# Optimization experiments

Hardware: AMD Instinct MI355X
Metric: run time of the kernel (lower is better)

Reference implementation:

```python
import jax, jax.numpy as jnp
import numpy as np

HALFKP = 64 * 5 * 64          # 20480
PAD = HALFKP                  # padding row index
L1, L2, L3 = 256, 31, 32
NB = 8                        # layer-stack / psqt buckets
EMB_DIM = L1 + NB             # 264


def setup_inputs() -> dict:
    key = jax.random.key(0)
    ks = jax.random.split(key, 16)
    B = 16384
    w_idx = jax.random.randint(ks[0], (B, 32), 0, HALFKP + 1)
    b_idx = jax.random.randint(ks[1], (B, 32), 0, HALFKP + 1)
    us = jax.random.uniform(ks[2], (B,), dtype=jnp.float32)
    them = jax.random.uniform(ks[3], (B,), dtype=jnp.float32)
    piece_count = jax.random.randint(ks[4], (B,), 2, 33)
    sigma = 0.025
    emb = jax.random.uniform(ks[5], (HALFKP + 1, EMB_DIM), jnp.float32, -sigma, sigma)
    emb = emb.at[PAD].set(0.0)
    def lin(k, out_f, in_f):
        bound = 1.0 / np.sqrt(in_f)
        k1, k2 = jax.random.split(k)
        W = jax.random.uniform(k1, (out_f, in_f), jnp.float32, -bound, bound)
        b = jax.random.uniform(k2, (out_f,), jnp.float32, -bound, bound)
        return W, b
    # StackedLinear init: replicate slot-0 weights across all buckets
    w1_0, b1_0 = lin(ks[6], L2 + 1, L1)
    w1 = jnp.tile(w1_0, (NB, 1)); b1 = jnp.tile(b1_0, NB)
    fw1 = jnp.zeros((L2 + 1, L1), jnp.float32)
    fb1 = jnp.zeros((L2 + 1,), jnp.float32)
    w2_0, b2_0 = lin(ks[7], L3, L2 * 2)
    w2 = jnp.tile(w2_0, (NB, 1)); b2 = jnp.tile(b2_0, NB)
    wo_0, _ = lin(ks[8], 1, L3)
    wo = jnp.tile(wo_0, (NB, 1)); bo = jnp.zeros((NB,), jnp.float32)
    return {"emb": emb, "w1": w1, "b1": b1, "fw1": fw1, "fb1": fb1,
            "w2": w2, "b2": b2, "wo": wo, "bo": bo,
            "us": us, "them": them,
            "w_idx": w_idx, "b_idx": b_idx, "piece_count": piece_count}


def reference(emb, w1, b1, fw1, fb1, w2, b2, wo, bo, us, them,
              w_idx, b_idx, piece_count):
    emb_eff = emb.at[PAD].set(0.0)                      # padding row contributes 0
    wp = emb_eff[w_idx].sum(axis=1)                     # [B, 264]
    bp = emb_eff[b_idx].sum(axis=1)
    w, wpsqt = wp[:, :L1], wp[:, L1:]
    b, bpsqt = bp[:, :L1], bp[:, L1:]
    us_c = us[:, None]; them_c = them[:, None]
    l0 = us_c * jnp.concatenate([w, b], 1) + them_c * jnp.concatenate([b, w], 1)
    l0 = jnp.clip(l0, 0.0, 1.0)                         # [B, 512]
    h = L1 // 2
    l0 = jnp.concatenate([l0[:, :h] * l0[:, h:2*h],
                          l0[:, 2*h:3*h] * l0[:, 3*h:]], 1) * (127.0 / 128.0)  # [B,256]
    bucket = jnp.clip((piece_count - 1) // 4, 0, 7)     # [B]
    # l1: factorized stacked linear, gather the bucket's slice only
    W1 = (w1 + jnp.tile(fw1, (NB, 1))).reshape(NB, L2 + 1, L1)
    B1 = (b1 + jnp.tile(fb1, NB)).reshape(NB, L2 + 1)
    l1c = jnp.einsum('bi,bji->bj', l0, W1[bucket]) + B1[bucket]   # [B,32]
    l1x, l1x_out = l1c[:, :L2], l1c[:, L2:]
    l1x = jnp.clip(jnp.concatenate([l1x * l1x * (255.0 / 256.0), l1x], 1), 0.0, 1.0)  # [B,62]
    W2 = w2.reshape(NB, L3, L2 * 2)
    l2x = jnp.clip(jnp.einsum('bi,bji->bj', l1x, W2[bucket]) + b2.reshape(NB, L3)[bucket], 0.0, 1.0)
    Wo = wo.reshape(NB, 1, L3)
    l3c = jnp.einsum('bi,bji->bj', l2x, Wo[bucket]) + bo.reshape(NB, 1)[bucket]       # [B,1]
    fc_out = l3c + l1x_out
    bk = bucket[:, None]
    psqt_out = (jnp.take_along_axis(wpsqt, bk, 1) - jnp.take_along_axis(bpsqt, bk, 1)) * (us_c - 0.5)
    return fc_out + psqt_out                            # [B,1]
```

## Files before the change

### kernel.cpp

```cpp
#include <hip/hip_runtime.h>

#define EMBD 264
#define NROWS 20481
#define NR4   5121
#define QS 5080.0f
#define INVQS (1.0f/5080.0f)

typedef short short8 __attribute__((ext_vector_type(8)));
typedef float f32x4  __attribute__((ext_vector_type(4)));

__device__ __forceinline__ float clamp01(float x) { return fminf(fmaxf(x, 0.f), 1.f); }
__device__ __forceinline__ unsigned short f2bf(float f) {
    unsigned u = __float_as_uint(f);
    u += 0x7fffu + ((u >> 16) & 1u);
    return (unsigned short)(u >> 16);
}

__global__ void prep_all(const float* __restrict__ emb, unsigned int* __restrict__ emb8,
                         float* __restrict__ psqt,
                         const float* __restrict__ w1, const float* __restrict__ fw1,
                         const float* __restrict__ b1, const float* __restrict__ fb1,
                         const float* __restrict__ w2,
                         unsigned short* __restrict__ w1b, float* __restrict__ b1c,
                         float* __restrict__ w2p) {
    if (blockIdx.x < NR4) {
        const int r = blockIdx.x * 4 + (threadIdx.x >> 6);
        const int t = threadIdx.x & 63;
        if (r >= NROWS) return;
        const bool pad = (r == NROWS - 1);
        const float4 v = *((const float4*)(emb + (size_t)r * EMBD) + t);
        int q0 = pad ? 128 : (int)rintf(v.x * QS) + 128;
        int q1 = pad ? 128 : (int)rintf(v.y * QS) + 128;
        int q2 = pad ? 128 : (int)rintf(v.z * QS) + 128;
        int q3 = pad ? 128 : (int)rintf(v.w * QS) + 128;
        q0 = min(max(q0, 0), 255); q1 = min(max(q1, 0), 255);
        q2 = min(max(q2, 0), 255); q3 = min(max(q3, 0), 255);
        emb8[(size_t)r * 64 + t] = (unsigned)q0 | ((unsigned)q1 << 8) |
                                   ((unsigned)q2 << 16) | ((unsigned)q3 << 24);
        if (t < 8) {
            float pv = emb[(size_t)r * EMBD + 256 + t];
            psqt[r * 8 + t] = pad ? 0.f : pv;
        }
    } else {
        const int e = (blockIdx.x - NR4) * 256 + threadIdx.x;
        const int bkt = e >> 13, rem = e & 8191;
        const int s = rem >> 10, rem2 = rem & 1023;
        const int nt = rem2 >> 9, rem3 = rem2 & 511;
        const int ln = rem3 >> 3, j = rem3 & 7;
        const int n  = nt * 16 + (ln & 15);
        const int hi = ln >> 4;
        const int k  = s * 32 + hi * 8 + j;
        const float v = w1[(bkt * 32 + n) * 256 + k] + fw1[n * 256 + k];
        w1b[e] = f2bf(v);
        if (e < 256) b1c[e] = b1[e] + fb1[e & 31];
        if (e < 16384) {
            const int jr = e >> 6, i = e & 63;
            float x = 0.f;
            if (i < 31) x = w2[jr * 62 + i];
            else if (i >= 32 && i < 63) x = w2[jr * 62 + i - 1];
            w2p[e] = x;
        }
    }
}

__global__ __launch_bounds__(512, 4) void nnue_fwd_mfma(
    const unsigned int* __restrict__ emb8,
    const float* __restrict__ psqt,
    const unsigned short* __restrict__ w1b,
    const float* __restrict__ b1c,
    const float* __restrict__ w2p,
    const float* __restrict__ b2,
    const float* __restrict__ wo,
    const float* __restrict__ bo,
    const float* __restrict__ us,
    const float* __restrict__ them,
    const int*   __restrict__ w_idx,
    const int*   __restrict__ b_idx,
    const int*   __restrict__ pcnt,
    float* __restrict__ out,
    int B)
{
    __shared__ unsigned short A_lds[16 * 280];
    __shared__ float l1c[8 * 16 * 36];
    __shared__ float psq_lds[16];
    __shared__ int   bkt_lds[16];

    const int tid  = threadIdx.x;
    const int lane = tid & 63;
    const int w    = tid >> 6;

    for (int rr = 0; rr < 2; ++rr) {
        const int m = w * 2 + rr;
        const int grow = __builtin_amdgcn_readfirstlane(blockIdx.x * 16 + m);

        const float usv = us[grow];
        const float thv = them[grow];
        int bucket = (pcnt[grow] - 1) >> 2;
        bucket = bucket > 7 ? 7 : bucket;
        bucket = __builtin_amdgcn_readfirstlane(bucket);

        const int* wrow = w_idx + grow * 32;
        const int* brow = b_idx + grow * 32;

        const int kk = lane & 31;
        const int pidx = (lane < 32) ? wrow[kk] : brow[kk];
        float ps = psqt[pidx * 8 + bucket];

        const unsigned M = 0x00FF00FFu;
        const unsigned loff = (unsigned)(lane << 2);
        const char* ebase = (const char*)emb8;

        unsigned vw[32], vb[32];
#pragma unroll
        for (int k = 0; k < 32; ++k) {
            const unsigned iw = (unsigned)__builtin_amdgcn_readfirstlane(wrow[k]);
            vw[k] = *(const unsigned*)(ebase + (size_t)((iw << 8) + loff));
        }
#pragma unroll
        for (int k = 0; k < 32; ++k) {
            const unsigned ib = (unsigned)__builtin_amdgcn_readfirstlane(brow[k]);
            vb[k] = *(const unsigned*)(ebase + (size_t)((ib << 8) + loff));
        }

        unsigned aw0a = 0, aw1a = 0, aw0b = 0, aw1b = 0;
#pragma unroll
        for (int k = 0; k < 32; k += 2) {
            aw0a += vw[k] & M;     aw1a += (vw[k] >> 8) & M;
            aw0b += vw[k+1] & M;   aw1b += (vw[k+1] >> 8) & M;
        }
        unsigned ab0a = 0, ab1a = 0, ab0b = 0, ab1b = 0;
#pragma unroll
        for (int k = 0; k < 32; k += 2) {
            ab0a += vb[k] & M;     ab1a += (vb[k] >> 8) & M;
            ab0b += vb[k+1] & M;   ab1b += (vb[k+1] >> 8) & M;
        }
        const unsigned aw0 = aw0a + aw0b, aw1 = aw1a + aw1b;
        const unsigned ab0 = ab0a + ab0b, ab1 = ab1a + ab1b;

        ps += __shfl_xor(ps, 16);
        ps += __shfl_xor(ps, 8);
        ps += __shfl_xor(ps, 4);
        ps += __shfl_xor(ps, 2);
        ps += __shfl_xor(ps, 1);
        const float psq_w = __shfl(ps, 0);
        const float psq_b = __shfl(ps, 32);

        float4 aw4, ab4;
        aw4.x = ((int)(aw0 & 0xffffu) - 4096) * INVQS;
        aw4.y = ((int)(aw1 & 0xffffu) - 4096) * INVQS;
        aw4.z = ((int)(aw0 >> 16)     - 4096) * INVQS;
        aw4.w = ((int)(aw1 >> 16)     - 4096) * INVQS;
        ab4.x = ((int)(ab0 & 0xffffu) - 4096) * INVQS;
        ab4.y = ((int)(ab1 & 0xffffu) - 4096) * INVQS;
        ab4.z = ((int)(ab0 >> 16)     - 4096) * INVQS;
        ab4.w = ((int)(ab1 >> 16)     - 4096) * INVQS;

        float4 p, q;
        p.x = clamp01(usv * aw4.x + thv * ab4.x);
        p.y = clamp01(usv * aw4.y + thv * ab4.y);
        p.z = clamp01(usv * aw4.z + thv * ab4.z);
        p.w = clamp01(usv * aw4.w + thv * ab4.w);
        q.x = clamp01(usv * ab4.x + thv * aw4.x);
        q.y = clamp01(usv * ab4.y + thv * aw4.y);
        q.z = clamp01(usv * ab4.z + thv * aw4.z);
        q.w = clamp01(usv * ab4.w + thv * aw4.w);

        float4 po, qo;
        po.x = __shfl_xor(p.x, 32); po.y = __shfl_xor(p.y, 32);
        po.z = __shfl_xor(p.z, 32); po.w = __shfl_xor(p.w, 32);
        qo.x = __shfl_xor(q.x, 32); qo.y = __shfl_xor(q.y, 32);
        qo.z = __shfl_xor(q.z, 32); qo.w = __shfl_xor(q.w, 32);
        const float c127 = 127.f / 128.f;
        float4 l0f;
        if (lane < 32) {
            l0f.x = p.x * po.x * c127; l0f.y = p.y * po.y * c127;
            l0f.z = p.z * po.z * c127; l0f.w = p.w * po.w * c127;
        } else {
            l0f.x = q.x * qo.x * c127; l0f.y = q.y * qo.y * c127;
            l0f.z = q.z * qo.z * c127; l0f.w = q.w * qo.w * c127;
        }

        const unsigned lo  = (unsigned)f2bf(l0f.x) | ((unsigned)f2bf(l0f.y) << 16);
        const unsigned hi2 = (unsigned)f2bf(l0f.z) | ((unsigned)f2bf(l0f.w) << 16);
        *((unsigned long long*)&A_lds[m * 280 + lane * 4]) =
            ((unsigned long long)hi2 << 32) | (unsigned long long)lo;
        if (lane == 0) {
            psq_lds[m] = (psq_w - psq_b) * (usv - 0.5f);
            bkt_lds[m] = bucket;
        }
    }
    __syncthreads();

    {
        const int col = lane & 15;
        const int hi  = lane >> 4;
        const int bkt = w;
        f32x4 acc[2];
        acc[0] = (f32x4){0.f, 0.f, 0.f, 0.f};
        acc[1] = (f32x4){0.f, 0.f, 0.f, 0.f};

#pragma unroll
        for (int s = 0; s < 8; ++s) {
            const short8 a = *((const short8*)&A_lds[col * 280 + s * 32 + hi * 8]);
#pragma unroll
            for (int nt = 0; nt < 2; ++nt) {
                const short8 bf = *((const short8*)&w1b[(((bkt * 8 + s) * 2 + nt) * 64 + lane) * 8]);
                acc[nt] = __builtin_amdgcn_mfma_f32_16x16x32_bf16(a, bf, acc[nt], 0, 0, 0);
            }
        }
#pragma unroll
        for (int nt = 0; nt < 2; ++nt) {
            const float bias = b1c[bkt * 32 + nt * 16 + col];
#pragma unroll
            for (int reg = 0; reg < 4; ++reg) {
                const int mr = hi * 4 + reg;
                l1c[(bkt * 16 + mr) * 36 + nt * 16 + col] = acc[nt][reg] + bias;
            }
        }
    }
    __syncthreads();

    if (tid < 256) {
        const int row = tid >> 4;
        const int jj  = tid & 15;
        const int bkt = bkt_lds[row];
        const float4* crow = (const float4*)&l1c[(bkt * 16 + row) * 36];
        float4 c4[8];
#pragma unroll
        for (int b5 = 0; b5 < 8; ++b5) c4[b5] = crow[b5];

        const float4* wr0 = (const float4*)&w2p[(bkt * 32 + jj) * 64];
        const float4* wr1 = (const float4*)&w2p[(bkt * 32 + jj + 16) * 64];
        float acc0 = 0.f, acc1 = 0.f;
        const float kq = 255.f / 256.f;
#pragma unroll
        for (int b5 = 0; b5 < 8; ++b5) {
            const float4 cv = c4[b5];
            float4 sq, ln;
            sq.x = clamp01(cv.x * cv.x * kq); ln.x = clamp01(cv.x);
            sq.y = clamp01(cv.y * cv.y * kq); ln.y = clamp01(cv.y);
            sq.z = clamp01(cv.z * cv.z * kq); ln.z = clamp01(cv.z);
            sq.w = clamp01(cv.w * cv.w * kq); ln.w = clamp01(cv.w);
            const float4 ws0 = wr0[b5], wl0 = wr0[8 + b5];
            const float4 ws1 = wr1[b5], wl1 = wr1[8 + b5];
            acc0 += sq.x * ws0.x + sq.y * ws0.y + sq.z * ws0.z + sq.w * ws0.w;
            acc0 += ln.x * wl0.x + ln.y * wl0.y + ln.z * wl0.z + ln.w * wl0.w;
            acc1 += sq.x * ws1.x + sq.y * ws1.y + sq.z * ws1.z + sq.w * ws1.w;
            acc1 += ln.x * wl1.x + ln.y * wl1.y + ln.z * wl1.z + ln.w * wl1.w;
        }
        const float t0 = clamp01(acc0 + b2[bkt * 32 + jj])      * wo[bkt * 32 + jj];
        const float t1 = clamp01(acc1 + b2[bkt * 32 + jj + 16]) * wo[bkt * 32 + jj + 16];
        float t = t0 + t1;
        t += __shfl_xor(t, 8);
        t += __shfl_xor(t, 4);
        t += __shfl_xor(t, 2);
        t += __shfl_xor(t, 1);
        if (jj == 0) {
            out[blockIdx.x * 16 + row] = t + bo[bkt] + c4[7].w + psq_lds[row];
        }
    }
}

__global__ __launch_bounds__(256) void nnue_fwd_f32(
    const float* __restrict__ emb,
    const float* __restrict__ w1e, const float* __restrict__ fw1,
    const float* __restrict__ b1e, const float* __restrict__ fb1,
    const float* __restrict__ w2,  const float* __restrict__ b2,
    const float* __restrict__ wo,  const float* __restrict__ bo,
    const float* __restrict__ us,  const float* __restrict__ them,
    const int* __restrict__ w_idx, const int* __restrict__ b_idx,
    const int* __restrict__ pcnt,  float* __restrict__ out, int B)
{
    const int lane = threadIdx.x & 63;
    const int row  = blockIdx.x * 4 + (threadIdx.x >> 6);
    if (row >= B) return;
    const float usv = us[row];
    const float thv = them[row];
    int bucket = (pcnt[row] - 1) >> 2;
    bucket = bucket > 7 ? 7 : bucket;
    bucket = __builtin_amdgcn_readfirstlane(bucket);
    const int kk = lane & 31;
    const int myidx = (lane < 32) ? w_idx[row * 32 + kk] : b_idx[row * 32 + kk];
    float ps = emb[(size_t)myidx * EMBD + 256 + bucket];
    ps += __shfl_xor(ps, 16); ps += __shfl_xor(ps, 8);
    ps += __shfl_xor(ps, 4);  ps += __shfl_xor(ps, 2); ps += __shfl_xor(ps, 1);
    const float psq_w = __shfl(ps, 0);
    const float psq_b = __shfl(ps, 32);
    float4 aw = make_float4(0,0,0,0), ab = make_float4(0,0,0,0);
#pragma unroll
    for (int k = 0; k < 32; ++k) {
        const int iw = __shfl(myidx, k);
        const int ib = __shfl(myidx, 32 + k);
        const float4 vw = *((const float4*)(emb + (size_t)iw * EMBD) + lane);
        const float4 vb = *((const float4*)(emb + (size_t)ib * EMBD) + lane);
        aw.x += vw.x; aw.y += vw.y; aw.z += vw.z; aw.w += vw.w;
        ab.x += vb.x; ab.y += vb.y; ab.z += vb.z; ab.w += vb.w;
    }
    float4 p, q;
    p.x = clamp01(usv*aw.x + thv*ab.x); p.y = clamp01(usv*aw.y + thv*ab.y);
    p.z = clamp01(usv*aw.z + thv*ab.z); p.w = clamp01(usv*aw.w + thv*ab.w);
    q.x = clamp01(usv*ab.x + thv*aw.x); q.y = clamp01(usv*ab.y + thv*aw.y);
    q.z = clamp01(usv*ab.z + thv*aw.z); q.w = clamp01(usv*ab.w + thv*aw.w);
    float4 po, qo;
    po.x = __shfl_xor(p.x,32); po.y = __shfl_xor(p.y,32);
    po.z = __shfl_xor(p.z,32); po.w = __shfl_xor(p.w,32);
    qo.x = __shfl_xor(q.x,32); qo.y = __shfl_xor(q.y,32);
    qo.z = __shfl_xor(q.z,32); qo.w = __shfl_xor(q.w,32);
    const float c127 = 127.f/128.f;
    float4 l0f;
    if (lane < 32) { l0f.x=p.x*po.x*c127; l0f.y=p.y*po.y*c127; l0f.z=p.z*po.z*c127; l0f.w=p.w*po.w*c127; }
    else           { l0f.x=q.x*qo.x*c127; l0f.y=q.y*qo.y*c127; l0f.z=q.z*qo.z*c127; l0f.w=q.w*qo.w*c127; }
    float part[32];
    const float4* w1p = (const float4*)(w1e + (size_t)bucket * 8192);
    const float4* f1p = (const float4*)fw1;
#pragma unroll
    for (int j = 0; j < 32; ++j) {
        float4 wv = w1p[j*64 + lane];
        float4 fv = f1p[j*64 + lane];
        wv.x+=fv.x; wv.y+=fv.y; wv.z+=fv.z; wv.w+=fv.w;
        part[j] = l0f.x*wv.x + l0f.y*wv.y + l0f.z*wv.z + l0f.w*wv.w;
    }
#pragma unroll
    for (int j = 0; j < 32; ++j) {
        float v = part[j];
        v += __shfl_xor(v,32); v += __shfl_xor(v,16); v += __shfl_xor(v,8);
        v += __shfl_xor(v,4);  v += __shfl_xor(v,2);  v += __shfl_xor(v,1);
        part[j] = v + b1e[bucket*32 + j] + fb1[j];
    }
    const float l1x_out = part[31];
    float acc2 = 0.f;
    if (lane < 32) {
        const float* w2r = w2 + (size_t)(bucket*32 + lane) * 62;
#pragma unroll
        for (int i = 0; i < 31; ++i) {
            const float a = part[i];
            acc2 += clamp01(a*a*(255.f/256.f)) * w2r[i];
            acc2 += clamp01(a) * w2r[31+i];
        }
        acc2 += b2[bucket*32 + lane];
        acc2 = clamp01(acc2) * wo[bucket*32 + lane];
    }
    acc2 += __shfl_xor(acc2,16); acc2 += __shfl_xor(acc2,8);
    acc2 += __shfl_xor(acc2,4);  acc2 += __shfl_xor(acc2,2); acc2 += __shfl_xor(acc2,1);
    if (lane == 0)
        out[row] = acc2 + bo[bucket] + l1x_out + (psq_w - psq_b) * (usv - 0.5f);
}

extern "C" void kernel_launch(void* const* d_in, const int* in_sizes, int n_in,
                              void* d_out, int out_size, void* d_ws, size_t ws_size,
                              hipStream_t stream) {
    const float* emb  = (const float*)d_in[0];
    const float* w1   = (const float*)d_in[1];
    const float* b1   = (const float*)d_in[2];
    const float* fw1  = (const float*)d_in[3];
    const float* fb1  = (const float*)d_in[4];
    const float* w2   = (const float*)d_in[5];
    const float* b2   = (const float*)d_in[6];
    const float* wo   = (const float*)d_in[7];
    const float* bo   = (const float*)d_in[8];
    const float* us   = (const float*)d_in[9];
    const float* them = (const float*)d_in[10];
    const int*   wi   = (const int*)d_in[11];
    const int*   bi   = (const int*)d_in[12];
    const int*   pc   = (const int*)d_in[13];
    float* out = (float*)d_out;

    const int B = in_sizes[9];

    const size_t emb8_bytes = (size_t)NROWS * 256;
    const size_t psqt_bytes = (size_t)NROWS * 8 * 4;
    const size_t w1b_bytes  = 65536 * 2;
    const size_t b1c_bytes  = 256 * 4;
    const size_t w2p_bytes  = 16384 * 4;
    const size_t need = emb8_bytes + psqt_bytes + w1b_bytes + b1c_bytes + w2p_bytes;

    if (ws_size >= need && (B % 16) == 0) {
        char* p = (char*)d_ws;
        unsigned int*   emb8 = (unsigned int*)p;     p += emb8_bytes;
        float*          psqt = (float*)p;            p += psqt_bytes;
        unsigned short* w1b  = (unsigned short*)p;   p += w1b_bytes;
        float*          b1c  = (float*)p;            p += b1c_bytes;
        float*          w2p  = (float*)p;

        prep_all<<<NR4 + 256, 256, 0, stream>>>(emb, emb8, psqt,
                                                w1, fw1, b1, fb1, w2, w1b, b1c, w2p);
        nnue_fwd_mfma<<<B / 16, 512, 0, stream>>>(emb8, psqt, w1b, b1c, w2p,
                                                  b2, wo, bo, us, them, wi, bi, pc, out, B);
    } else {
        nnue_fwd_f32<<<(B + 3) / 4, 256, 0, stream>>>(emb, w1, fw1, b1, fb1,
                                                      w2, b2, wo, bo, us, them, wi, bi, pc, out, B);
    }
}
```

Measured before the change: 139.5 us.

## Gather embedding rows with 16-byte loads split across lane groups

Replaces 64 scalar 4-byte gathers per row (one per feature, all lanes on one embedding row) with 16 vectorized 16-byte loads. Each 16-lane group fetches a different feature row, and partial sums are then reduced across groups with cross-lane shuffles. This cuts the number of load instructions and the number of readfirstlane index reads. The l0 pairing shuffle and the LDS store index are remapped to the new lane-to-element layout. In exchange it adds shuffle-reduction and select overhead.

```diff
diff --git a/kernel.cpp b/kernel.cpp
--- a/kernel.cpp
+++ b/kernel.cpp
@@ -89,6 +89,10 @@
     const int lane = tid & 63;
     const int w    = tid >> 6;
 
+    const int t = lane & 15;
+    const int g = lane >> 4;
+    const int d = (t << 2) + g;
+
     for (int rr = 0; rr < 2; ++rr) {
         const int m = w * 2 + rr;
         const int grow = __builtin_amdgcn_readfirstlane(blockIdx.x * 16 + m);
@@ -103,39 +107,54 @@
         const int* brow = b_idx + grow * 32;
 
         const int kk = lane & 31;
-        const int pidx = (lane < 32) ? wrow[kk] : brow[kk];
-        float ps = psqt[pidx * 8 + bucket];
+        const int iv = (lane < 32) ? wrow[kk] : brow[kk];
+
+        float ps = psqt[(size_t)iv * 8 + bucket];
+
+        uint4 vws[8], vbs[8];
+#pragma unroll
+        for (int k = 0; k < 8; ++k) {
+            const int rw = __shfl(iv, (k << 2) + g);
+            vws[k] = *(const uint4*)((const char*)emb8 +
+                                     (((unsigned)rw << 8) + (unsigned)(t << 4)));
+        }
+#pragma unroll
+        for (int k = 0; k < 8; ++k) {
+            const int rb = __shfl(iv, 32 + (k << 2) + g);
+            vbs[k] = *(const uint4*)((const char*)emb8 +
+                                     (((unsigned)rb << 8) + (unsigned)(t << 4)));
+        }
 
         const unsigned M = 0x00FF00FFu;
-        const unsigned loff = (unsigned)(lane << 2);
-        const char* ebase = (const char*)emb8;
-
-        unsigned vw[32], vb[32];
-#pragma unroll
-        for (int k = 0; k < 32; ++k) {
-            const unsigned iw = (unsigned)__builtin_amdgcn_readfirstlane(wrow[k]);
-            vw[k] = *(const unsigned*)(ebase + (size_t)((iw << 8) + loff));
-        }
-#pragma unroll
-        for (int k = 0; k < 32; ++k) {
-            const unsigned ib = (unsigned)__builtin_amdgcn_readfirstlane(brow[k]);
-            vb[k] = *(const unsigned*)(ebase + (size_t)((ib << 8) + loff));
-        }
-
-        unsigned aw0a = 0, aw1a = 0, aw0b = 0, aw1b = 0;
-#pragma unroll
-        for (int k = 0; k < 32; k += 2) {
-            aw0a += vw[k] & M;     aw1a += (vw[k] >> 8) & M;
-            aw0b += vw[k+1] & M;   aw1b += (vw[k+1] >> 8) & M;
-        }
-        unsigned ab0a = 0, ab1a = 0, ab0b = 0, ab1b = 0;
-#pragma unroll
-        for (int k = 0; k < 32; k += 2) {
-            ab0a += vb[k] & M;     ab1a += (vb[k] >> 8) & M;
-            ab0b += vb[k+1] & M;   ab1b += (vb[k+1] >> 8) & M;
-        }
-        const unsigned aw0 = aw0a + aw0b, aw1 = aw1a + aw1b;
-        const unsigned ab0 = ab0a + ab0b, ab1 = ab1a + ab1b;
+        unsigned a0w[4] = {0,0,0,0}, a1w[4] = {0,0,0,0};
+        unsigned a0b[4] = {0,0,0,0}, a1b[4] = {0,0,0,0};
+#pragma unroll
+        for (int k = 0; k < 8; ++k) {
+            a0w[0] += vws[k].x & M;  a1w[0] += (vws[k].x >> 8) & M;
+            a0w[1] += vws[k].y & M;  a1w[1] += (vws[k].y >> 8) & M;
+            a0w[2] += vws[k].z & M;  a1w[2] += (vws[k].z >> 8) & M;
+            a0w[3] += vws[k].w & M;  a1w[3] += (vws[k].w >> 8) & M;
+        }
+#pragma unroll
+        for (int k = 0; k < 8; ++k) {
+            a0b[0] += vbs[k].x & M;  a1b[0] += (vbs[k].x >> 8) & M;
+            a0b[1] += vbs[k].y & M;  a1b[1] += (vbs[k].y >> 8) & M;
+            a0b[2] += vbs[k].z & M;  a1b[2] += (vbs[k].z >> 8) & M;
+            a0b[3] += vbs[k].w & M;  a1b[3] += (vbs[k].w >> 8) & M;
+        }
+
+#pragma unroll
+        for (int j = 0; j < 4; ++j) {
+            a0w[j] += __shfl_xor(a0w[j], 16);  a0w[j] += __shfl_xor(a0w[j], 32);
+            a1w[j] += __shfl_xor(a1w[j], 16);  a1w[j] += __shfl_xor(a1w[j], 32);
+            a0b[j] += __shfl_xor(a0b[j], 16);  a0b[j] += __shfl_xor(a0b[j], 32);
+            a1b[j] += __shfl_xor(a1b[j], 16);  a1b[j] += __shfl_xor(a1b[j], 32);
+        }
+        const bool gl = (g & 1) != 0, gh = (g & 2) != 0;
+        const unsigned aw0 = gh ? (gl ? a0w[3] : a0w[2]) : (gl ? a0w[1] : a0w[0]);
+        const unsigned aw1 = gh ? (gl ? a1w[3] : a1w[2]) : (gl ? a1w[1] : a1w[0]);
+        const unsigned ab0 = gh ? (gl ? a0b[3] : a0b[2]) : (gl ? a0b[1] : a0b[0]);
+        const unsigned ab1 = gh ? (gl ? a1b[3] : a1b[2]) : (gl ? a1b[1] : a1b[0]);
 
         ps += __shfl_xor(ps, 16);
         ps += __shfl_xor(ps, 8);
@@ -166,13 +185,13 @@
         q.w = clamp01(usv * ab4.w + thv * aw4.w);
 
         float4 po, qo;
-        po.x = __shfl_xor(p.x, 32); po.y = __shfl_xor(p.y, 32);
-        po.z = __shfl_xor(p.z, 32); po.w = __shfl_xor(p.w, 32);
-        qo.x = __shfl_xor(q.x, 32); qo.y = __shfl_xor(q.y, 32);
-        qo.z = __shfl_xor(q.z, 32); qo.w = __shfl_xor(q.w, 32);
+        po.x = __shfl_xor(p.x, 8); po.y = __shfl_xor(p.y, 8);
+        po.z = __shfl_xor(p.z, 8); po.w = __shfl_xor(p.w, 8);
+        qo.x = __shfl_xor(q.x, 8); qo.y = __shfl_xor(q.y, 8);
+        qo.z = __shfl_xor(q.z, 8); qo.w = __shfl_xor(q.w, 8);
         const float c127 = 127.f / 128.f;
         float4 l0f;
-        if (lane < 32) {
+        if (t < 8) {
             l0f.x = p.x * po.x * c127; l0f.y = p.y * po.y * c127;
             l0f.z = p.z * po.z * c127; l0f.w = p.w * po.w * c127;
         } else {
@@ -182,7 +201,7 @@
 
         const unsigned lo  = (unsigned)f2bf(l0f.x) | ((unsigned)f2bf(l0f.y) << 16);
         const unsigned hi2 = (unsigned)f2bf(l0f.z) | ((unsigned)f2bf(l0f.w) << 16);
-        *((unsigned long long*)&A_lds[m * 280 + lane * 4]) =
+        *((unsigned long long*)&A_lds[m * 280 + d * 4]) =
             ((unsigned long long)hi2 << 32) | (unsigned long long)lo;
         if (lane == 0) {
             psq_lds[m] = (psq_w - psq_b) * (usv - 0.5f);
@@ -250,13 +269,13 @@
         }
         const float t0 = clamp01(acc0 + b2[bkt * 32 + jj])      * wo[bkt * 32 + jj];
         const float t1 = clamp01(acc1 + b2[bkt * 32 + jj + 16]) * wo[bkt * 32 + jj + 16];
-        float t = t0 + t1;
-        t += __shfl_xor(t, 8);
-        t += __shfl_xor(t, 4);
-        t += __shfl_xor(t, 2);
-        t += __shfl_xor(t, 1);
+        float tsum = t0 + t1;
+        tsum += __shfl_xor(tsum, 8);
+        tsum += __shfl_xor(tsum, 4);
+        tsum += __shfl_xor(tsum, 2);
+        tsum += __shfl_xor(tsum, 1);
         if (jj == 0) {
-            out[blockIdx.x * 16 + row] = t + bo[bkt] + c4[7].w + psq_lds[row];
+            out[blockIdx.x * 16 + row] = tsum + bo[bkt] + c4[7].w + psq_lds[row];
         }
     }
 }
```

After: 137.7 us. About the same (-1.3%).
